# Optimization experiments

Measured on AMD Instinct MI355X. Metric: run time of the kernel, lower is better.

The kernel has to match this reference:

```python
import jax, jax.numpy as jnp
import numpy as np
from jax import lax

B, C, HID, H, W = 8, 256, 64, 64, 64

def conv3x3(x, w, b):
    # x: [B,C_in,H,W], w: [C_out,C_in,3,3], b: [C_out]
    y = lax.conv_general_dilated(x, w, window_strides=(1, 1), padding='SAME',
                                 dimension_numbers=('NCHW', 'OIHW', 'NCHW'))
    return y + b[None, :, None, None]

def setup_inputs() -> dict:
    key = jax.random.key(0)
    ks = jax.random.split(key, 7)
    s_in = 1.0 / np.sqrt(C * 9)
    return {
        'x': jax.random.normal(ks[0], (B, C, H, W), dtype=jnp.float32),
        'Wq': jax.random.normal(ks[1], (HID, C, 3, 3), dtype=jnp.float32) * s_in,
        'bq': jax.random.normal(ks[2], (HID,), dtype=jnp.float32) * s_in,
        'Wk': jax.random.normal(ks[3], (HID, C, 3, 3), dtype=jnp.float32) * s_in,
        'bk': jax.random.normal(ks[4], (HID,), dtype=jnp.float32) * s_in,
        'Wv': jax.random.normal(ks[5], (C, C, 3, 3), dtype=jnp.float32) * s_in,
        'bv': jax.random.normal(ks[6], (C,), dtype=jnp.float32) * s_in,
    }

def reference(x, Wq, bq, Wk, bk, Wv, bv):
    b, c, w, h = x.shape
    n = w * h
    q = conv3x3(x, Wq, bq).reshape(b, -1, n).transpose(0, 2, 1)  # [B,N,hid]
    k = conv3x3(x, Wk, bk).reshape(b, -1, n)                      # [B,hid,N]
    v = conv3x3(x, Wv, bv).reshape(b, c, n)                       # [B,C,N]
    attn = jax.nn.softmax(jnp.einsum('bnd,bdm->bnm', q, k), axis=-1)  # [B,N,N]
    # out = bmm(value, attn^T): out[b,c,m] = sum_n v[b,c,n] * attn[b,m,n]
    out = jnp.einsum('bcn,bmn->bcm', v, attn).reshape(b, c, w, h)
    # F.interpolate(out, h, mode='bilinear') with H==W is an exact identity
    return out + x
```

## Files before the change

kernel.cpp:

```cpp
#include <hip/hip_runtime.h>
#include <math.h>

#define NB   8
#define NC   256
#define ND   64
#define NPIX 4096
#define LSTR 72

typedef short bf16x8 __attribute__((ext_vector_type(8)));
typedef float f32x4  __attribute__((ext_vector_type(4)));
typedef float f32x16 __attribute__((ext_vector_type(16)));

static __device__ __forceinline__ ushort f2bf(float f) {
    uint u = __float_as_uint(f);
    u += 0x7fffu + ((u >> 16) & 1u);
    return (ushort)(u >> 16);
}
static __device__ __forceinline__ float bf2f(ushort h) {
    return __uint_as_float(((uint)h) << 16);
}

__global__ __launch_bounds__(256) void transpose_x(
    const float* __restrict__ x, ushort* __restrict__ xth, ushort* __restrict__ xtl)
{
    __shared__ float tile[64][68];
    const int t = threadIdx.x;
    const int p0 = blockIdx.x * 64, c0 = blockIdx.y * 64, b = blockIdx.z;

    const int cl = t >> 4, p4 = (t & 15) * 4;
    #pragma unroll
    for (int i = 0; i < 4; i++) {
        const int c = cl + 16 * i;
        *(float4*)&tile[c][p4] =
            *(const float4*)&x[((size_t)(b * NC + c0 + c)) * NPIX + p0 + p4];
    }
    __syncthreads();

    const int pl = t & 63, ch = t >> 6;
    float v[16];
    #pragma unroll
    for (int j = 0; j < 16; j++) v[j] = tile[ch * 16 + j][pl];
    ushort h[16], l[16];
    #pragma unroll
    for (int j = 0; j < 16; j++) {
        h[j] = f2bf(v[j]);
        l[j] = f2bf(v[j] - bf2f(h[j]));
    }
    const size_t o = ((size_t)(b * NPIX + p0 + pl)) * 256 + c0 + ch * 16;
    *(uint4*)&xth[o]     = *(uint4*)&h[0];
    *(uint4*)&xth[o + 8] = *(uint4*)&h[8];
    *(uint4*)&xtl[o]     = *(uint4*)&l[0];
    *(uint4*)&xtl[o + 8] = *(uint4*)&l[8];
}

__global__ __launch_bounds__(256) void transpose_w(
    const float* __restrict__ Wq, const float* __restrict__ Wk,
    const float* __restrict__ Wv,
    ushort* __restrict__ qh, ushort* __restrict__ ql,
    ushort* __restrict__ kh, ushort* __restrict__ kl,
    ushort* __restrict__ vh)
{
    __shared__ float wb[2304];
    const int g = blockIdx.x, t = threadIdx.x;
    const float* src;
    ushort *dh, *dl;
    int co, Co, split;
    if (g < 64)       { src = Wq + (size_t)g * 2304; co = g;       Co = 64;  dh = qh; dl = ql; split = 1; }
    else if (g < 128) { src = Wk + (size_t)(g - 64) * 2304; co = g - 64; Co = 64; dh = kh; dl = kl; split = 1; }
    else              { src = Wv + (size_t)(g - 128) * 2304; co = g - 128; Co = 256; dh = vh; dl = nullptr; split = 0; }

    for (int i = t; i < 2304; i += 256) wb[i] = src[i];
    __syncthreads();
    for (int j = t; j < 2304; j += 256) {
        const int rs = j >> 8, ci = j & 255;
        const float v = wb[ci * 9 + rs];
        const ushort hv = f2bf(v);
        const size_t o = ((size_t)(rs * Co + co)) * 256 + ci;
        dh[o] = hv;
        if (split) dl[o] = f2bf(v - bf2f(hv));
    }
}

__global__ __launch_bounds__(256) void conv_split_k(
    const ushort* __restrict__ xth, const ushort* __restrict__ xtl,
    const ushort* __restrict__ wqh, const ushort* __restrict__ wql,
    const ushort* __restrict__ wkh, const ushort* __restrict__ wkl,
    const float* __restrict__ bq, const float* __restrict__ bk,
    ushort* __restrict__ qoh, ushort* __restrict__ qol,
    ushort* __restrict__ koh, ushort* __restrict__ kol)
{
    extern __shared__ char smem[];
    ushort* xsh = (ushort*)smem;
    ushort* xsl = xsh + 6 * 66 * 24;
    ushort* wsp = xsl + 6 * 66 * 24;
    float*  sbias = (float*)(wsp + 9 * 64 * 24);

    const int hq = blockIdx.x, b = blockIdx.y, ct = blockIdx.z;
    const ushort* wth = ct ? wkh : wqh;
    const ushort* wtl = ct ? wkl : wql;
    const float*  bias = ct ? bk : bq;
    ushort* outh = ct ? koh : qoh;
    ushort* outl = ct ? kol : qol;

    const int t = threadIdx.x;
    const int wv = t >> 6, lane = t & 63;
    const int l31 = lane & 31, khl = lane >> 5;
    const int lanebase = l31 * 24 + khl * 8;
    const int h = hq * 4 + wv;

    if (t < 64) sbias[t] = bias[t];
    for (int i = t; i < 384; i += 256) {
        const int p = i / 192, r2 = i % 192;
        const int row = r2 / 32, e = (r2 % 32) / 16, ci = r2 & 15;
        (p ? xsl : xsh)[(row * 66 + e * 65) * 24 + ci] = 0;
    }

    f32x16 a00 = {0}, a01 = {0}, a10 = {0}, a11 = {0};

    for (int ch = 0; ch < 16; ch++) {
        __syncthreads();
        const int ci0 = ch * 16;
        #pragma unroll
        for (int pl2 = 0; pl2 < 2; pl2++) {
            const ushort* src = pl2 ? xtl : xth;
            ushort* dst = pl2 ? xsl : xsh;
            #pragma unroll
            for (int i = 0; i < 3; i++) {
                const int a = i * 256 + t;
                const int cih = a & 1, col = (a >> 1) & 63, row = a >> 7;
                const int hs = hq * 4 + row - 1;
                uint4 val = {0, 0, 0, 0};
                if (hs >= 0 && hs < 64)
                    val = *(const uint4*)&src[((size_t)(b * NPIX + hs * 64 + col)) * 256 + ci0 + cih * 8];
                *(uint4*)&dst[(row * 66 + 1 + col) * 24 + cih * 8] = val;
            }
        }
        #pragma unroll
        for (int i = 0; i < 5; i++) {
            const int a = i * 256 + t;
            if (a < 1152) {
                const int cih = a & 1, co = (a >> 1) & 63, rs = a >> 7;
                uint4 wv4 = *(const uint4*)&wth[((size_t)(rs * 64 + co)) * 256 + ci0 + cih * 8];
                *(uint4*)&wsp[(rs * 64 + co) * 24 + cih * 8] = wv4;
            }
        }
        __syncthreads();
        #pragma unroll
        for (int rs = 0; rs < 9; rs++) {
            const int r = rs / 3, s = rs % 3;
            bf16x8 A0 = *(const bf16x8*)&wsp[rs * 1536 + lanebase];
            bf16x8 A1 = *(const bf16x8*)&wsp[rs * 1536 + 768 + lanebase];
            const int xo = ((wv + r) * 66 + s) * 24 + lanebase;
            bf16x8 B0h = *(const bf16x8*)&xsh[xo];
            bf16x8 B1h = *(const bf16x8*)&xsh[xo + 768];
            bf16x8 B0l = *(const bf16x8*)&xsl[xo];
            bf16x8 B1l = *(const bf16x8*)&xsl[xo + 768];
            a00 = __builtin_amdgcn_mfma_f32_32x32x16_bf16(A0, B0h, a00, 0, 0, 0);
            a01 = __builtin_amdgcn_mfma_f32_32x32x16_bf16(A0, B1h, a01, 0, 0, 0);
            a10 = __builtin_amdgcn_mfma_f32_32x32x16_bf16(A1, B0h, a10, 0, 0, 0);
            a11 = __builtin_amdgcn_mfma_f32_32x32x16_bf16(A1, B1h, a11, 0, 0, 0);
            a00 = __builtin_amdgcn_mfma_f32_32x32x16_bf16(A0, B0l, a00, 0, 0, 0);
            a01 = __builtin_amdgcn_mfma_f32_32x32x16_bf16(A0, B1l, a01, 0, 0, 0);
            a10 = __builtin_amdgcn_mfma_f32_32x32x16_bf16(A1, B0l, a10, 0, 0, 0);
            a11 = __builtin_amdgcn_mfma_f32_32x32x16_bf16(A1, B1l, a11, 0, 0, 0);
        }
        __syncthreads();
        #pragma unroll
        for (int i = 0; i < 5; i++) {
            const int a = i * 256 + t;
            if (a < 1152) {
                const int cih = a & 1, co = (a >> 1) & 63, rs = a >> 7;
                uint4 wv4 = *(const uint4*)&wtl[((size_t)(rs * 64 + co)) * 256 + ci0 + cih * 8];
                *(uint4*)&wsp[(rs * 64 + co) * 24 + cih * 8] = wv4;
            }
        }
        __syncthreads();
        #pragma unroll
        for (int rs = 0; rs < 9; rs++) {
            const int r = rs / 3, s = rs % 3;
            bf16x8 A0 = *(const bf16x8*)&wsp[rs * 1536 + lanebase];
            bf16x8 A1 = *(const bf16x8*)&wsp[rs * 1536 + 768 + lanebase];
            const int xo = ((wv + r) * 66 + s) * 24 + lanebase;
            bf16x8 B0h = *(const bf16x8*)&xsh[xo];
            bf16x8 B1h = *(const bf16x8*)&xsh[xo + 768];
            a00 = __builtin_amdgcn_mfma_f32_32x32x16_bf16(A0, B0h, a00, 0, 0, 0);
            a01 = __builtin_amdgcn_mfma_f32_32x32x16_bf16(A0, B1h, a01, 0, 0, 0);
            a10 = __builtin_amdgcn_mfma_f32_32x32x16_bf16(A1, B0h, a10, 0, 0, 0);
            a11 = __builtin_amdgcn_mfma_f32_32x32x16_bf16(A1, B1h, a11, 0, 0, 0);
        }
    }

    const float4* sb4 = (const float4*)sbias;
    #pragma unroll
    for (int ms = 0; ms < 2; ms++)
        #pragma unroll
        for (int ns = 0; ns < 2; ns++) {
            const f32x16 av = ms ? (ns ? a11 : a10) : (ns ? a01 : a00);
            const int p = h * 64 + ns * 32 + l31;
            #pragma unroll
            for (int g = 0; g < 4; g++) {
                const float4 bi = sb4[ms * 8 + 2 * g + khl];
                float v0 = av[4 * g + 0] + bi.x;
                float v1 = av[4 * g + 1] + bi.y;
                float v2 = av[4 * g + 2] + bi.z;
                float v3 = av[4 * g + 3] + bi.w;
                ushort4 hv, lv;
                hv.x = f2bf(v0); lv.x = f2bf(v0 - bf2f(hv.x));
                hv.y = f2bf(v1); lv.y = f2bf(v1 - bf2f(hv.y));
                hv.z = f2bf(v2); lv.z = f2bf(v2 - bf2f(hv.z));
                hv.w = f2bf(v3); lv.w = f2bf(v3 - bf2f(hv.w));
                const size_t o = ((size_t)(b * NPIX + p)) * 64 + ms * 32 + 8 * g + 4 * khl;
                *(ushort4*)&outh[o] = hv;
                *(ushort4*)&outl[o] = lv;
            }
        }
}

__global__ __launch_bounds__(256) void conv_v_k(
    const ushort* __restrict__ xth, const ushort* __restrict__ wtv,
    const float* __restrict__ bv, ushort* __restrict__ vout)
{
    extern __shared__ char smem[];
    ushort* xsh = (ushort*)smem;
    ushort* wsp = xsh + 6 * 66 * 24;
    float*  sbias = (float*)(wsp + 9 * 64 * 24);

    const int hq = blockIdx.x, b = blockIdx.y, co0 = blockIdx.z * 64;
    const int t = threadIdx.x;
    const int wv = t >> 6, lane = t & 63;
    const int l31 = lane & 31, khl = lane >> 5;
    const int lanebase = l31 * 24 + khl * 8;
    const int h = hq * 4 + wv;

    if (t < 64) sbias[t] = bv[co0 + t];
    for (int i = t; i < 192; i += 256) {
        const int row = i / 32, e = (i % 32) / 16, ci = i & 15;
        xsh[(row * 66 + e * 65) * 24 + ci] = 0;
    }

    f32x16 a00 = {0}, a01 = {0}, a10 = {0}, a11 = {0};

    for (int ch = 0; ch < 16; ch++) {
        __syncthreads();
        const int ci0 = ch * 16;
        #pragma unroll
        for (int i = 0; i < 3; i++) {
            const int a = i * 256 + t;
            const int cih = a & 1, col = (a >> 1) & 63, row = a >> 7;
            const int hs = hq * 4 + row - 1;
            uint4 val = {0, 0, 0, 0};
            if (hs >= 0 && hs < 64)
                val = *(const uint4*)&xth[((size_t)(b * NPIX + hs * 64 + col)) * 256 + ci0 + cih * 8];
            *(uint4*)&xsh[(row * 66 + 1 + col) * 24 + cih * 8] = val;
        }
        #pragma unroll
        for (int i = 0; i < 5; i++) {
            const int a = i * 256 + t;
            if (a < 1152) {
                const int cih = a & 1, co = (a >> 1) & 63, rs = a >> 7;
                uint4 wv4 = *(const uint4*)&wtv[((size_t)(rs * 256 + co0 + co)) * 256 + ci0 + cih * 8];
                *(uint4*)&wsp[(rs * 64 + co) * 24 + cih * 8] = wv4;
            }
        }
        __syncthreads();
        #pragma unroll
        for (int rs = 0; rs < 9; rs++) {
            const int r = rs / 3, s = rs % 3;
            const int xo = ((wv + r) * 66 + s) * 24 + lanebase;
            bf16x8 A0 = *(const bf16x8*)&xsh[xo];
            bf16x8 A1 = *(const bf16x8*)&xsh[xo + 768];
            bf16x8 B0 = *(const bf16x8*)&wsp[rs * 1536 + lanebase];
            bf16x8 B1 = *(const bf16x8*)&wsp[rs * 1536 + 768 + lanebase];
            a00 = __builtin_amdgcn_mfma_f32_32x32x16_bf16(A0, B0, a00, 0, 0, 0);
            a01 = __builtin_amdgcn_mfma_f32_32x32x16_bf16(A0, B1, a01, 0, 0, 0);
            a10 = __builtin_amdgcn_mfma_f32_32x32x16_bf16(A1, B0, a10, 0, 0, 0);
            a11 = __builtin_amdgcn_mfma_f32_32x32x16_bf16(A1, B1, a11, 0, 0, 0);
        }
    }

    #pragma unroll
    for (int ns = 0; ns < 2; ns++) {
        const int co = co0 + ns * 32 + l31;
        const float bi = sbias[ns * 32 + l31];
        #pragma unroll
        for (int ms = 0; ms < 2; ms++) {
            const f32x16 av = ms ? (ns ? a11 : a10) : (ns ? a01 : a00);
            #pragma unroll
            for (int g = 0; g < 4; g++) {
                const int p = h * 64 + ms * 32 + 8 * g + 4 * khl;
                ushort4 ov;
                ov.x = f2bf(av[4 * g + 0] + bi);
                ov.y = f2bf(av[4 * g + 1] + bi);
                ov.z = f2bf(av[4 * g + 2] + bi);
                ov.w = f2bf(av[4 * g + 3] + bi);
                *(ushort4*)&vout[((size_t)(b * NC + co)) * NPIX + p] = ov;
            }
        }
    }
}

__global__ __launch_bounds__(256, 2) void attn_k(
    const ushort* __restrict__ qh, const ushort* __restrict__ ql,
    const ushort* __restrict__ kh, const ushort* __restrict__ kl,
    const ushort* __restrict__ vb, const float* __restrict__ x,
    float* __restrict__ out)
{
    const int id = blockIdx.x;
    const int b  = id & 7;
    const int m0 = (id >> 3) * 64;
    const int t  = threadIdx.x;
    const int w  = t >> 6;
    const int lane = t & 63;
    const int quad = lane >> 4;
    const int l16  = lane & 15;

    __shared__ ushort sps[2][64 * LSTR];
    __shared__ float  red[4][64];
    __shared__ float  ivl[64];

    bf16x8 aqh[4][2], aql[4][2];
    #pragma unroll
    for (int mg = 0; mg < 4; mg++)
        #pragma unroll
        for (int ks = 0; ks < 2; ks++) {
            const size_t g = ((size_t)b * NPIX + m0 + mg * 16 + l16) * ND + ks * 32 + quad * 8;
            aqh[mg][ks] = *(const bf16x8*)&qh[g];
            aql[mg][ks] = *(const bf16x8*)&ql[g];
        }

    const size_t kbase = ((size_t)b * NPIX + 16 * w + l16) * ND + quad * 8;
    size_t vbase[4];
    #pragma unroll
    for (int ct = 0; ct < 4; ct++)
        vbase[ct] = ((size_t)b * NC + 64 * w + ct * 16 + l16) * NPIX + quad * 8;

    bf16x8 kfh[2], kfl[2], vf[4][2];
    #pragma unroll
    for (int ks = 0; ks < 2; ks++) {
        kfh[ks] = *(const bf16x8*)&kh[kbase + ks * 32];
        kfl[ks] = *(const bf16x8*)&kl[kbase + ks * 32];
    }
    #pragma unroll
    for (int ct = 0; ct < 4; ct++)
        #pragma unroll
        for (int ks = 0; ks < 2; ks++)
            vf[ct][ks] = *(const bf16x8*)&vb[vbase[ct] + ks * 32];

    f32x4 acc[4][4];
    #pragma unroll
    for (int i = 0; i < 4; i++)
        #pragma unroll
        for (int j = 0; j < 4; j++) acc[i][j] = (f32x4){0.f, 0.f, 0.f, 0.f};
    float lsum[4] = {0.f, 0.f, 0.f, 0.f};

    for (int n0 = 0; n0 < NPIX; n0 += 64) {
        const int buf = (n0 >> 6) & 1;
        const bool nxt = (n0 + 64) < NPIX;

        #pragma unroll
        for (int mg = 0; mg < 4; mg++) {
            f32x4 s = {0.f, 0.f, 0.f, 0.f};
            #pragma unroll
            for (int ks = 0; ks < 2; ks++) {
                s = __builtin_amdgcn_mfma_f32_16x16x32_bf16(kfh[ks], aqh[mg][ks], s, 0, 0, 0);
                s = __builtin_amdgcn_mfma_f32_16x16x32_bf16(kfl[ks], aqh[mg][ks], s, 0, 0, 0);
                s = __builtin_amdgcn_mfma_f32_16x16x32_bf16(kfh[ks], aql[mg][ks], s, 0, 0, 0);
            }
            uint2 pk;
            {
                const ushort p0 = f2bf(__expf(s[0] - 30.f));
                const ushort p1 = f2bf(__expf(s[1] - 30.f));
                const ushort p2 = f2bf(__expf(s[2] - 30.f));
                const ushort p3 = f2bf(__expf(s[3] - 30.f));
                lsum[mg] += (bf2f(p0) + bf2f(p1)) + (bf2f(p2) + bf2f(p3));
                pk.x = (uint)p0 | ((uint)p1 << 16);
                pk.y = (uint)p2 | ((uint)p3 << 16);
            }
            *(uint2*)&sps[buf][(mg * 16 + l16) * LSTR + 16 * w + quad * 4] = pk;
        }

        if (nxt) {
            const size_t kb = kbase + (size_t)(n0 + 64) * ND;
            #pragma unroll
            for (int ks = 0; ks < 2; ks++) {
                kfh[ks] = *(const bf16x8*)&kh[kb + ks * 32];
                kfl[ks] = *(const bf16x8*)&kl[kb + ks * 32];
            }
        }

        asm volatile("s_waitcnt lgkmcnt(0)\n\ts_barrier" ::: "memory");

        __builtin_amdgcn_s_setprio(1);
        #pragma unroll
        for (int ks = 0; ks < 2; ks++) {
            bf16x8 ap[4];
            #pragma unroll
            for (int mg = 0; mg < 4; mg++)
                ap[mg] = *(const bf16x8*)&sps[buf][(mg * 16 + l16) * LSTR + ks * 32 + quad * 8];
            #pragma unroll
            for (int mg = 0; mg < 4; mg++)
                #pragma unroll
                for (int ct = 0; ct < 4; ct++)
                    acc[mg][ct] = __builtin_amdgcn_mfma_f32_16x16x32_bf16(
                        ap[mg], vf[ct][ks], acc[mg][ct], 0, 0, 0);
        }
        __builtin_amdgcn_s_setprio(0);

        if (nxt) {
            #pragma unroll
            for (int ct = 0; ct < 4; ct++)
                #pragma unroll
                for (int ks = 0; ks < 2; ks++)
                    vf[ct][ks] = *(const bf16x8*)&vb[vbase[ct] + n0 + 64 + ks * 32];
        }
    }

    #pragma unroll
    for (int mg = 0; mg < 4; mg++) {
        lsum[mg] += __shfl_xor(lsum[mg], 16, 64);
        lsum[mg] += __shfl_xor(lsum[mg], 32, 64);
    }
    if (quad == 0) {
        #pragma unroll
        for (int mg = 0; mg < 4; mg++) red[w][mg * 16 + l16] = lsum[mg];
    }
    __syncthreads();
    if (t < 64)
        ivl[t] = 1.f / (red[0][t] + red[1][t] + red[2][t] + red[3][t]);
    __syncthreads();

    #pragma unroll
    for (int mg = 0; mg < 4; mg++) {
        const int mrow = mg * 16 + quad * 4;
        const float4 il4 = *(const float4*)&ivl[mrow];
        const int m = m0 + mrow;
        #pragma unroll
        for (int ct = 0; ct < 4; ct++) {
            const int c = 64 * w + ct * 16 + l16;
            const size_t base = ((size_t)b * NC + c) * NPIX + m;
            const float4 xv = *(const float4*)&x[base];
            const f32x4 a = acc[mg][ct];
            float4 o;
            o.x = fmaf(a[0], il4.x, xv.x);
            o.y = fmaf(a[1], il4.y, xv.y);
            o.z = fmaf(a[2], il4.z, xv.z);
            o.w = fmaf(a[3], il4.w, xv.w);
            *(float4*)&out[base] = o;
        }
    }
}

extern "C" void kernel_launch(void* const* d_in, const int* in_sizes, int n_in,
                              void* d_out, int out_size, void* d_ws, size_t ws_size,
                              hipStream_t stream)
{
    const float* x  = (const float*)d_in[0];
    const float* Wq = (const float*)d_in[1];
    const float* bq = (const float*)d_in[2];
    const float* Wk = (const float*)d_in[3];
    const float* bk = (const float*)d_in[4];
    const float* Wv = (const float*)d_in[5];
    const float* bv = (const float*)d_in[6];
    float* outp = (float*)d_out;

    const size_t XT = (size_t)NB * NPIX * 256;
    const size_t QK = (size_t)NB * NPIX * ND;
    ushort* xt_h = (ushort*)d_ws;
    ushort* xt_l = xt_h + XT;
    ushort* v_b  = xt_l;
    ushort* q_h  = xt_l + XT;
    ushort* q_l  = q_h + QK;
    ushort* k_h  = q_l + QK;
    ushort* k_l  = k_h + QK;
    ushort* wtq_h = k_l + QK;
    ushort* wtq_l = wtq_h + 147456;
    ushort* wtk_h = wtq_l + 147456;
    ushort* wtk_l = wtk_h + 147456;
    ushort* wtv_h = wtk_l + 147456;

    dim3 blk(256);
    transpose_x<<<dim3(64, 4, NB), blk, 0, stream>>>(x, xt_h, xt_l);
    transpose_w<<<dim3(384), blk, 0, stream>>>(Wq, Wk, Wv, wtq_h, wtq_l, wtk_h, wtk_l, wtv_h);
    conv_split_k<<<dim3(16, NB, 2), blk, 65920, stream>>>(
        xt_h, xt_l, wtq_h, wtq_l, wtk_h, wtk_l, bq, bk, q_h, q_l, k_h, k_l);
    conv_v_k<<<dim3(16, NB, 4), blk, 46912, stream>>>(xt_h, wtv_h, bv, v_b);
    attn_k<<<dim3(512), blk, 0, stream>>>(q_h, q_l, k_h, k_l, v_b, x, outp);
}
```

Before: 424.8 us.

## Software-pipeline QK/exp of next tile with PV MFMAs and swizzle P tile LDS

Restructures the attention loop so the QK^T scores and exponentials for the next key tile are computed into the other LDS buffer while the current tile's P·V MFMAs run. K fragments are prefetched two tiles ahead. The padded LDS stride is replaced by an XOR swizzle on a 128-byte row to avoid bank conflicts without padding. The s_setprio hints are dropped, and register pressure rises from holding two P fragment sets plus the prefetched K.

```diff
diff --git a/kernel.cpp b/kernel.cpp
--- a/kernel.cpp
+++ b/kernel.cpp
@@ -5,7 +5,6 @@
 #define NC   256
 #define ND   64
 #define NPIX 4096
-#define LSTR 72
 
 typedef short bf16x8 __attribute__((ext_vector_type(8)));
 typedef float f32x4  __attribute__((ext_vector_type(4)));
@@ -314,7 +313,7 @@
     const int quad = lane >> 4;
     const int l16  = lane & 15;
 
-    __shared__ ushort sps[2][64 * LSTR];
+    __shared__ ushort sps[2][64 * 64];
     __shared__ float  red[4][64];
     __shared__ float  ivl[64];
 
@@ -353,10 +352,7 @@
         for (int j = 0; j < 4; j++) acc[i][j] = (f32x4){0.f, 0.f, 0.f, 0.f};
     float lsum[4] = {0.f, 0.f, 0.f, 0.f};
 
-    for (int n0 = 0; n0 < NPIX; n0 += 64) {
-        const int buf = (n0 >> 6) & 1;
-        const bool nxt = (n0 + 64) < NPIX;
-
+    auto qk_tile = [&](int obuf) {
         #pragma unroll
         for (int mg = 0; mg < 4; mg++) {
             f32x4 s = {0.f, 0.f, 0.f, 0.f};
@@ -366,46 +362,64 @@
                 s = __builtin_amdgcn_mfma_f32_16x16x32_bf16(kfl[ks], aqh[mg][ks], s, 0, 0, 0);
                 s = __builtin_amdgcn_mfma_f32_16x16x32_bf16(kfh[ks], aql[mg][ks], s, 0, 0, 0);
             }
+            const ushort p0 = f2bf(__expf(s[0] - 30.f));
+            const ushort p1 = f2bf(__expf(s[1] - 30.f));
+            const ushort p2 = f2bf(__expf(s[2] - 30.f));
+            const ushort p3 = f2bf(__expf(s[3] - 30.f));
+            lsum[mg] += (bf2f(p0) + bf2f(p1)) + (bf2f(p2) + bf2f(p3));
             uint2 pk;
-            {
-                const ushort p0 = f2bf(__expf(s[0] - 30.f));
-                const ushort p1 = f2bf(__expf(s[1] - 30.f));
-                const ushort p2 = f2bf(__expf(s[2] - 30.f));
-                const ushort p3 = f2bf(__expf(s[3] - 30.f));
-                lsum[mg] += (bf2f(p0) + bf2f(p1)) + (bf2f(p2) + bf2f(p3));
-                pk.x = (uint)p0 | ((uint)p1 << 16);
-                pk.y = (uint)p2 | ((uint)p3 << 16);
-            }
-            *(uint2*)&sps[buf][(mg * 16 + l16) * LSTR + 16 * w + quad * 4] = pk;
-        }
-
-        if (nxt) {
-            const size_t kb = kbase + (size_t)(n0 + 64) * ND;
-            #pragma unroll
-            for (int ks = 0; ks < 2; ks++) {
-                kfh[ks] = *(const bf16x8*)&kh[kb + ks * 32];
-                kfl[ks] = *(const bf16x8*)&kl[kb + ks * 32];
-            }
-        }
-
-        asm volatile("s_waitcnt lgkmcnt(0)\n\ts_barrier" ::: "memory");
-
-        __builtin_amdgcn_s_setprio(1);
+            pk.x = (uint)p0 | ((uint)p1 << 16);
+            pk.y = (uint)p2 | ((uint)p3 << 16);
+            const int row = mg * 16 + l16;
+            const int bo = (32 * w + quad * 8) ^ ((row & 7) << 4);
+            *(uint2*)((char*)&sps[obuf][0] + row * 128 + bo) = pk;
+        }
+    };
+
+    qk_tile(0);
+    {
+        const size_t kb = kbase + (size_t)64 * ND;
         #pragma unroll
         for (int ks = 0; ks < 2; ks++) {
-            bf16x8 ap[4];
-            #pragma unroll
-            for (int mg = 0; mg < 4; mg++)
-                ap[mg] = *(const bf16x8*)&sps[buf][(mg * 16 + l16) * LSTR + ks * 32 + quad * 8];
+            kfh[ks] = *(const bf16x8*)&kh[kb + ks * 32];
+            kfl[ks] = *(const bf16x8*)&kl[kb + ks * 32];
+        }
+    }
+    asm volatile("s_waitcnt lgkmcnt(0)\n\ts_barrier" ::: "memory");
+
+    for (int n0 = 0; n0 < NPIX; n0 += 64) {
+        const int buf = (n0 >> 6) & 1;
+        const bool nxt = (n0 + 64) < NPIX;
+
+        bf16x8 ap[2][4];
+        #pragma unroll
+        for (int ks = 0; ks < 2; ks++)
+            #pragma unroll
+            for (int mg = 0; mg < 4; mg++) {
+                const int row = mg * 16 + l16;
+                const int bo = (ks * 64 + quad * 16) ^ ((row & 7) << 4);
+                ap[ks][mg] = *(const bf16x8*)((const char*)&sps[buf][0] + row * 128 + bo);
+            }
+
+        if (nxt) qk_tile(buf ^ 1);
+
+        #pragma unroll
+        for (int ks = 0; ks < 2; ks++)
             #pragma unroll
             for (int mg = 0; mg < 4; mg++)
                 #pragma unroll
                 for (int ct = 0; ct < 4; ct++)
                     acc[mg][ct] = __builtin_amdgcn_mfma_f32_16x16x32_bf16(
-                        ap[mg], vf[ct][ks], acc[mg][ct], 0, 0, 0);
-        }
-        __builtin_amdgcn_s_setprio(0);
-
+                        ap[ks][mg], vf[ct][ks], acc[mg][ct], 0, 0, 0);
+
+        if (n0 + 128 < NPIX) {
+            const size_t kb = kbase + (size_t)(n0 + 128) * ND;
+            #pragma unroll
+            for (int ks = 0; ks < 2; ks++) {
+                kfh[ks] = *(const bf16x8*)&kh[kb + ks * 32];
+                kfl[ks] = *(const bf16x8*)&kl[kb + ks * 32];
+            }
+        }
         if (nxt) {
             #pragma unroll
             for (int ct = 0; ct < 4; ct++)
@@ -413,6 +427,8 @@
                 for (int ks = 0; ks < 2; ks++)
                     vf[ct][ks] = *(const bf16x8*)&vb[vbase[ct] + n0 + 64 + ks * 32];
         }
+
+        asm volatile("s_waitcnt lgkmcnt(0)\n\ts_barrier" ::: "memory");
     }
 
     #pragma unroll
```

New measurement: 424.0 us. About the same (-0.2%).

## Register-prefetch next channel chunk in conv kernels and merge hi/lo weight staging

Applied to the files above, without the earlier changes.

Both conv kernels now issue the global loads for the next input-channel chunk into registers before running the MFMA loop on the current chunk, then write them to shared memory between two barriers. The split-precision Q/K conv stages both hi and lo weight tiles at once in a larger LDS buffer, cutting the per-chunk barrier count in half. Address math is hoisted out of the loop. This trades extra registers and LDS (limiting occupancy, with launch bounds set accordingly) for hiding global load latency behind compute.

```diff
diff --git a/kernel.cpp b/kernel.cpp
--- a/kernel.cpp
+++ b/kernel.cpp
@@ -81,7 +81,7 @@
     }
 }
 
-__global__ __launch_bounds__(256) void conv_split_k(
+__global__ __launch_bounds__(256, 1) void conv_split_k(
     const ushort* __restrict__ xth, const ushort* __restrict__ xtl,
     const ushort* __restrict__ wqh, const ushort* __restrict__ wql,
     const ushort* __restrict__ wkh, const ushort* __restrict__ wkl,
@@ -91,9 +91,9 @@
 {
     extern __shared__ char smem[];
     ushort* xsh = (ushort*)smem;
-    ushort* xsl = xsh + 6 * 66 * 24;
-    ushort* wsp = xsl + 6 * 66 * 24;
-    float*  sbias = (float*)(wsp + 9 * 64 * 24);
+    ushort* xsl = xsh + 9504;
+    ushort* wsp = xsl + 9504;
+    float*  sbias = (float*)(wsp + 2 * 13824);
 
     const int hq = blockIdx.x, b = blockIdx.y, ct = blockIdx.z;
     const ushort* wth = ct ? wkh : wqh;
@@ -110,41 +110,77 @@
 
     if (t < 64) sbias[t] = bias[t];
     for (int i = t; i < 384; i += 256) {
-        const int p = i / 192, r2 = i % 192;
-        const int row = r2 / 32, e = (r2 % 32) / 16, ci = r2 & 15;
+        const int p = (i >= 192), r2 = i - 192 * p;
+        const int row = r2 >> 5, e = (r2 & 31) >> 4, ci = r2 & 15;
         (p ? xsl : xsh)[(row * 66 + e * 65) * 24 + ci] = 0;
     }
 
+    uint xg[3], xlds[3];
+    bool xval[3];
+    #pragma unroll
+    for (int i = 0; i < 3; i++) {
+        const int a = i * 256 + t;
+        const int cih = a & 1, col = (a >> 1) & 63, row = a >> 7;
+        const int hs = hq * 4 + row - 1;
+        xval[i] = (hs >= 0 && hs < 64);
+        const int hc = xval[i] ? hs : 0;
+        xg[i]   = (uint)(((b * NPIX + hc * 64 + col)) * 256 + cih * 8);
+        xlds[i] = (uint)((row * 66 + 1 + col) * 24 + cih * 8);
+    }
+    uint wg[5], wlds[5];
+    #pragma unroll
+    for (int i = 0; i < 5; i++) {
+        const int a = i * 256 + t;
+        const int aa = (a < 1152) ? a : 0;
+        const int cih = aa & 1, co = (aa >> 1) & 63, rs = aa >> 7;
+        wg[i]   = (uint)((rs * 64 + co) * 256 + cih * 8);
+        wlds[i] = (uint)((rs * 64 + co) * 24 + cih * 8);
+    }
+    const bool w4 = (1024 + t) < 1152;
+
+    uint4 xr[2][3], wr[2][5];
+    #define LOADST(ci0)                                                        \
+    {                                                                          \
+        _Pragma("unroll")                                                      \
+        for (int i = 0; i < 3; i++) {                                          \
+            xr[0][i] = xval[i] ? *(const uint4*)&xth[xg[i] + (ci0)]            \
+                               : (uint4){0, 0, 0, 0};                          \
+            xr[1][i] = xval[i] ? *(const uint4*)&xtl[xg[i] + (ci0)]            \
+                               : (uint4){0, 0, 0, 0};                          \
+        }                                                                      \
+        _Pragma("unroll")                                                      \
+        for (int i = 0; i < 5; i++) {                                          \
+            if (i < 4 || w4) {                                                 \
+                wr[0][i] = *(const uint4*)&wth[wg[i] + (ci0)];                 \
+                wr[1][i] = *(const uint4*)&wtl[wg[i] + (ci0)];                 \
+            }                                                                  \
+        }                                                                      \
+    }
+    #define WRITEST()                                                          \
+    {                                                                          \
+        _Pragma("unroll")                                                      \
+        for (int i = 0; i < 3; i++) {                                          \
+            *(uint4*)&xsh[xlds[i]] = xr[0][i];                                 \
+            *(uint4*)&xsl[xlds[i]] = xr[1][i];                                 \
+        }                                                                      \
+        _Pragma("unroll")                                                      \
+        for (int i = 0; i < 5; i++) {                                          \
+            if (i < 4 || w4) {                                                 \
+                *(uint4*)&wsp[wlds[i]]         = wr[0][i];                     \
+                *(uint4*)&wsp[13824 + wlds[i]] = wr[1][i];                     \
+            }                                                                  \
+        }                                                                      \
+    }
+
     f32x16 a00 = {0}, a01 = {0}, a10 = {0}, a11 = {0};
 
+    LOADST(0);
+    WRITEST();
+    asm volatile("s_waitcnt lgkmcnt(0)\n\ts_barrier" ::: "memory");
+
     for (int ch = 0; ch < 16; ch++) {
-        __syncthreads();
-        const int ci0 = ch * 16;
-        #pragma unroll
-        for (int pl2 = 0; pl2 < 2; pl2++) {
-            const ushort* src = pl2 ? xtl : xth;
-            ushort* dst = pl2 ? xsl : xsh;
-            #pragma unroll
-            for (int i = 0; i < 3; i++) {
-                const int a = i * 256 + t;
-                const int cih = a & 1, col = (a >> 1) & 63, row = a >> 7;
-                const int hs = hq * 4 + row - 1;
-                uint4 val = {0, 0, 0, 0};
-                if (hs >= 0 && hs < 64)
-                    val = *(const uint4*)&src[((size_t)(b * NPIX + hs * 64 + col)) * 256 + ci0 + cih * 8];
-                *(uint4*)&dst[(row * 66 + 1 + col) * 24 + cih * 8] = val;
-            }
-        }
-        #pragma unroll
-        for (int i = 0; i < 5; i++) {
-            const int a = i * 256 + t;
-            if (a < 1152) {
-                const int cih = a & 1, co = (a >> 1) & 63, rs = a >> 7;
-                uint4 wv4 = *(const uint4*)&wth[((size_t)(rs * 64 + co)) * 256 + ci0 + cih * 8];
-                *(uint4*)&wsp[(rs * 64 + co) * 24 + cih * 8] = wv4;
-            }
-        }
-        __syncthreads();
+        if (ch < 15) LOADST((ch + 1) * 16);
+
         #pragma unroll
         for (int rs = 0; rs < 9; rs++) {
             const int r = rs / 3, s = rs % 3;
@@ -164,22 +200,11 @@
             a10 = __builtin_amdgcn_mfma_f32_32x32x16_bf16(A1, B0l, a10, 0, 0, 0);
             a11 = __builtin_amdgcn_mfma_f32_32x32x16_bf16(A1, B1l, a11, 0, 0, 0);
         }
-        __syncthreads();
-        #pragma unroll
-        for (int i = 0; i < 5; i++) {
-            const int a = i * 256 + t;
-            if (a < 1152) {
-                const int cih = a & 1, co = (a >> 1) & 63, rs = a >> 7;
-                uint4 wv4 = *(const uint4*)&wtl[((size_t)(rs * 64 + co)) * 256 + ci0 + cih * 8];
-                *(uint4*)&wsp[(rs * 64 + co) * 24 + cih * 8] = wv4;
-            }
-        }
-        __syncthreads();
         #pragma unroll
         for (int rs = 0; rs < 9; rs++) {
             const int r = rs / 3, s = rs % 3;
-            bf16x8 A0 = *(const bf16x8*)&wsp[rs * 1536 + lanebase];
-            bf16x8 A1 = *(const bf16x8*)&wsp[rs * 1536 + 768 + lanebase];
+            bf16x8 A0 = *(const bf16x8*)&wsp[13824 + rs * 1536 + lanebase];
+            bf16x8 A1 = *(const bf16x8*)&wsp[13824 + rs * 1536 + 768 + lanebase];
             const int xo = ((wv + r) * 66 + s) * 24 + lanebase;
             bf16x8 B0h = *(const bf16x8*)&xsh[xo];
             bf16x8 B1h = *(const bf16x8*)&xsh[xo + 768];
@@ -188,7 +213,15 @@
             a10 = __builtin_amdgcn_mfma_f32_32x32x16_bf16(A1, B0h, a10, 0, 0, 0);
             a11 = __builtin_amdgcn_mfma_f32_32x32x16_bf16(A1, B1h, a11, 0, 0, 0);
         }
-    }
+
+        if (ch < 15) {
+            asm volatile("s_waitcnt lgkmcnt(0)\n\ts_barrier" ::: "memory");
+            WRITEST();
+            asm volatile("s_waitcnt lgkmcnt(0)\n\ts_barrier" ::: "memory");
+        }
+    }
+    #undef LOADST
+    #undef WRITEST
 
     const float4* sb4 = (const float4*)sbias;
     #pragma unroll
@@ -216,14 +249,14 @@
         }
 }
 
-__global__ __launch_bounds__(256) void conv_v_k(
+__global__ __launch_bounds__(256, 2) void conv_v_k(
     const ushort* __restrict__ xth, const ushort* __restrict__ wtv,
     const float* __restrict__ bv, ushort* __restrict__ vout)
 {
     extern __shared__ char smem[];
     ushort* xsh = (ushort*)smem;
-    ushort* wsp = xsh + 6 * 66 * 24;
-    float*  sbias = (float*)(wsp + 9 * 64 * 24);
+    ushort* wsp = xsh + 9504;
+    float*  sbias = (float*)(wsp + 13824);
 
     const int hq = blockIdx.x, b = blockIdx.y, co0 = blockIdx.z * 64;
     const int t = threadIdx.x;
@@ -234,35 +267,62 @@
 
     if (t < 64) sbias[t] = bv[co0 + t];
     for (int i = t; i < 192; i += 256) {
-        const int row = i / 32, e = (i % 32) / 16, ci = i & 15;
+        const int row = i >> 5, e = (i & 31) >> 4, ci = i & 15;
         xsh[(row * 66 + e * 65) * 24 + ci] = 0;
     }
 
+    uint xg[3], xlds[3];
+    bool xval[3];
+    #pragma unroll
+    for (int i = 0; i < 3; i++) {
+        const int a = i * 256 + t;
+        const int cih = a & 1, col = (a >> 1) & 63, row = a >> 7;
+        const int hs = hq * 4 + row - 1;
+        xval[i] = (hs >= 0 && hs < 64);
+        const int hc = xval[i] ? hs : 0;
+        xg[i]   = (uint)(((b * NPIX + hc * 64 + col)) * 256 + cih * 8);
+        xlds[i] = (uint)((row * 66 + 1 + col) * 24 + cih * 8);
+    }
+    uint wg[5], wlds[5];
+    #pragma unroll
+    for (int i = 0; i < 5; i++) {
+        const int a = i * 256 + t;
+        const int aa = (a < 1152) ? a : 0;
+        const int cih = aa & 1, co = (aa >> 1) & 63, rs = aa >> 7;
+        wg[i]   = (uint)((rs * 256 + co0 + co) * 256 + cih * 8);
+        wlds[i] = (uint)((rs * 64 + co) * 24 + cih * 8);
+    }
+    const bool w4 = (1024 + t) < 1152;
+
+    uint4 xr[3], wr[5];
+    #define LOADV(ci0)                                                         \
+    {                                                                          \
+        _Pragma("unroll")                                                      \
+        for (int i = 0; i < 3; i++)                                            \
+            xr[i] = xval[i] ? *(const uint4*)&xth[xg[i] + (ci0)]               \
+                            : (uint4){0, 0, 0, 0};                             \
+        _Pragma("unroll")                                                      \
+        for (int i = 0; i < 5; i++)                                            \
+            if (i < 4 || w4) wr[i] = *(const uint4*)&wtv[wg[i] + (ci0)];       \
+    }
+    #define WRITEV()                                                           \
+    {                                                                          \
+        _Pragma("unroll")                                                      \
+        for (int i = 0; i < 3; i++) *(uint4*)&xsh[xlds[i]] = xr[i];            \
+        _Pragma("unroll")                                                      \
+        for (int i = 0; i < 5; i++)                                            \
+            if (i < 4 || w4) *(uint4*)&wsp[wlds[i]] = wr[i];                   \
+    }
+
     f32x16 a00 = {0}, a01 = {0}, a10 = {0}, a11 = {0};
 
+    LOADV(0);
+    WRITEV();
+    asm volatile("s_waitcnt lgkmcnt(0)\n\ts_barrier" ::: "memory");
+
     for (int ch = 0; ch < 16; ch++) {
-        __syncthreads();
-        const int ci0 = ch * 16;
-        #pragma unroll
-        for (int i = 0; i < 3; i++) {
-            const int a = i * 256 + t;
-            const int cih = a & 1, col = (a >> 1) & 63, row = a >> 7;
-            const int hs = hq * 4 + row - 1;
-            uint4 val = {0, 0, 0, 0};
-            if (hs >= 0 && hs < 64)
-                val = *(const uint4*)&xth[((size_t)(b * NPIX + hs * 64 + col)) * 256 + ci0 + cih * 8];
-            *(uint4*)&xsh[(row * 66 + 1 + col) * 24 + cih * 8] = val;
-        }
-        #pragma unroll
-        for (int i = 0; i < 5; i++) {
-            const int a = i * 256 + t;
-            if (a < 1152) {
-                const int cih = a & 1, co = (a >> 1) & 63, rs = a >> 7;
-                uint4 wv4 = *(const uint4*)&wtv[((size_t)(rs * 256 + co0 + co)) * 256 + ci0 + cih * 8];
-                *(uint4*)&wsp[(rs * 64 + co) * 24 + cih * 8] = wv4;
-            }
-        }
-        __syncthreads();
+        if (ch < 15) LOADV((ch + 1) * 16);
+
         #pragma unroll
         for (int rs = 0; rs < 9; rs++) {
             const int r = rs / 3, s = rs % 3;
@@ -276,7 +336,15 @@
             a10 = __builtin_amdgcn_mfma_f32_32x32x16_bf16(A1, B0, a10, 0, 0, 0);
             a11 = __builtin_amdgcn_mfma_f32_32x32x16_bf16(A1, B1, a11, 0, 0, 0);
         }
-    }
+
+        if (ch < 15) {
+            asm volatile("s_waitcnt lgkmcnt(0)\n\ts_barrier" ::: "memory");
+            WRITEV();
+            asm volatile("s_waitcnt lgkmcnt(0)\n\ts_barrier" ::: "memory");
+        }
+    }
+    #undef LOADV
+    #undef WRITEV
 
     #pragma unroll
     for (int ns = 0; ns < 2; ns++) {
@@ -481,7 +549,7 @@
     dim3 blk(256);
     transpose_x<<<dim3(64, 4, NB), blk, 0, stream>>>(x, xt_h, xt_l);
     transpose_w<<<dim3(384), blk, 0, stream>>>(Wq, Wk, Wv, wtq_h, wtq_l, wtk_h, wtk_l, wtv_h);
-    conv_split_k<<<dim3(16, NB, 2), blk, 65920, stream>>>(
+    conv_split_k<<<dim3(16, NB, 2), blk, 93568, stream>>>(
         xt_h, xt_l, wtq_h, wtq_l, wtk_h, wtk_l, bq, bk, q_h, q_l, k_h, k_l);
     conv_v_k<<<dim3(16, NB, 4), blk, 46912, stream>>>(xt_h, wtv_h, bv, v_b);
     attn_k<<<dim3(512), blk, 0, stream>>>(q_h, q_l, k_h, k_l, v_b, x, outp);
```

New measurement: 466.7 us. 1.1x slower.
